# Kernel tuning notes

Measured on AMD Instinct MI355X. Metric: run time of the kernel, lower is better.

## Reference

```python
import jax, jax.numpy as jnp
import numpy as np

L = 32          # ss_num: number of sampled layers
D = 512         # lstm_size
OPS = 16        # operations_num
TEMP = 5.0
TANH_C = 2.5
OP_TANH_RED = 2.5
NEG = jnp.float32(-1e9)  # finite mask value (avoids inf/nan in grads)


def setup_inputs() -> dict:
    key = jax.random.key(0)
    ks = jax.random.split(key, 9)
    u = lambda k, s: jax.random.uniform(k, s, jnp.float32, -0.1, 0.1)  # reset_param: uniform(-0.1, 0.1)
    return {
        "embedding": u(ks[0], (OPS + 1, D)),
        "w_ih": u(ks[1], (4 * D, D)),
        "w_hh": u(ks[2], (4 * D, D)),
        "b_ih": u(ks[3], (4 * D,)),
        "b_hh": u(ks[4], (4 * D,)),
        "w_attn_1": u(ks[5], (D, D)),
        "w_attn_2": u(ks[6], (D, D)),
        "index_fc": u(ks[7], (D,)),
        "op_fc": u(ks[8], (OPS, D)),
    }


def _lstm_cell(x, h, c, w_ih, w_hh, b_ih, b_hh):
    # torch.nn.LSTMCell: gate order i, f, g, o
    g = x @ w_ih.T + b_ih + h @ w_hh.T + b_hh
    i, f, gg, o = jnp.split(g, 4, axis=-1)
    c2 = jax.nn.sigmoid(f) * c + jax.nn.sigmoid(i) * jnp.tanh(gg)
    h2 = jax.nn.sigmoid(o) * jnp.tanh(c2)
    return h2, c2


def reference(embedding, w_ih, w_hh, b_ih, b_hh, w_attn_1, w_attn_2, index_fc, op_fc):
    cell = lambda x, h, c: _lstm_cell(x, h, c, w_ih, w_hh, b_ih, b_hh)
    skey = jax.random.key(42)

    # --- initial construct_node (prev state = zeros) ---
    inp0 = embedding[OPS]                 # embedding of sentinel token [D]
    h, c = cell(inp0, jnp.zeros((D,), jnp.float32), jnp.zeros((D,), jnp.float32))
    anchors = jnp.zeros((L + 1, D), jnp.float32)            # anchor[0] = zeros_like(h)
    anchors_w1 = jnp.zeros((L + 1, D), jnp.float32).at[0].set(h @ w_attn_1.T)

    def step(carry, t):
        h, c, inp, anchors, anchors_w1, key = carry
        k1, k2, key = jax.random.split(key, 3)
        valid = jnp.arange(L + 1) <= t  # anchors 0..t exist at layer t

        # node selection
        h, c = cell(inp, h, c)
        query = jnp.tanh(anchors_w1 + h @ w_attn_2.T)        # [L+1, D]
        idx_logits = (query @ index_fc) / TEMP               # [L+1]
        idx_logits = TANH_C * jnp.tanh(idx_logits)
        idx_logits = jnp.where(valid, idx_logits, NEG)
        node_idx = jax.random.categorical(k1, idx_logits)
        lsm = jax.nn.log_softmax(idx_logits)
        node_lp = -lsm[node_idx]                             # cross_entropy
        node_ent = -jnp.sum(jnp.where(valid, lsm, 0.0) * jnp.exp(lsm))

        # op selection
        op_in = anchors[node_idx]
        h, c = cell(op_in, h, c)
        op_logits = (h @ op_fc.T) / TEMP
        op_logits = (TANH_C / OP_TANH_RED) * jnp.tanh(op_logits)
        op_idx = jax.random.categorical(k2, op_logits)
        olsm = jax.nn.log_softmax(op_logits)
        op_lp = -olsm[op_idx]
        op_ent = -jnp.sum(olsm * jnp.exp(olsm))

        inp = embedding[op_idx]
        anchors = anchors.at[t + 1].set(h)
        anchors_w1 = anchors_w1.at[t + 1].set(h @ w_attn_1.T)
        ent = jax.lax.stop_gradient(node_ent + op_ent)       # entropy is .detach()ed
        return (h, c, inp, anchors, anchors_w1, key), (node_idx, op_idx, node_lp + op_lp, ent)

    carry0 = (h, c, inp0, anchors, anchors_w1, skey)
    _, (nidx, oidx, lps, ents) = jax.lax.scan(step, carry0, jnp.arange(L))
    arch_seq = jnp.stack([nidx, oidx], axis=1).reshape(-1)   # interleave [node, op] x L
    return arch_seq, jnp.sum(ents), jnp.sum(lps)
```

## Files before the change

### kernel.cpp

```cpp
#include <hip/hip_runtime.h>
#include <stdint.h>


#define KWG    64
#define NTH    512
#define LSTEPS 32
#define DDIM   512
#define NOPS   16
#define NEGC   (-1.0e9f)

static __device__ __forceinline__ void tf2x32(uint32_t k0, uint32_t k1,
                                              uint32_t c0, uint32_t c1,
                                              uint32_t& o0, uint32_t& o1){
  uint32_t ks2 = k0 ^ k1 ^ 0x1BD11BDAu;
  uint32_t x0 = c0 + k0;
  uint32_t x1 = c1 + k1;
#define TFR(r) { x0 += x1; x1 = (x1 << (r)) | (x1 >> (32 - (r))); x1 ^= x0; }
  TFR(13) TFR(15) TFR(26) TFR(6)
  x0 += k1;  x1 += ks2 + 1u;
  TFR(17) TFR(29) TFR(16) TFR(24)
  x0 += ks2; x1 += k0 + 2u;
  TFR(13) TFR(15) TFR(26) TFR(6)
  x0 += k0;  x1 += k1 + 3u;
  TFR(17) TFR(29) TFR(16) TFR(24)
  x0 += k1;  x1 += ks2 + 4u;
  TFR(13) TFR(15) TFR(26) TFR(6)
  x0 += ks2; x1 += k0 + 5u;
#undef TFR
  o0 = x0; o1 = x1;
}

static __device__ __forceinline__ float gumbel_bits(uint32_t bits){
  float f = __uint_as_float((bits >> 9) | 0x3f800000u) - 1.0f;
  float u = (f == 0.0f) ? 1.1754943508222875e-38f : f;
  return -logf(-logf(u));
}

static __device__ __forceinline__ float sigm(float x){
  return 1.0f / (1.0f + expf(-x));
}

static __device__ __forceinline__ float wredsum(float v){
  #pragma unroll
  for (int m = 32; m; m >>= 1) v += __shfl_xor(v, m, 64);
  return v;
}

static __device__ __forceinline__ void gl8(const float* __restrict__ p, int lane, float* r){
  #pragma unroll
  for (int k = 0; k < 8; ++k) r[k] = p[(k << 6) + lane];
}

static __device__ __forceinline__ float dot8(const float* w, const float* x){
  float s = 0.f;
  #pragma unroll
  for (int k = 0; k < 8; ++k) s += w[k]*x[k];
  return s;
}

static __device__ __forceinline__ uint64_t tpack(uint32_t tag, float f){
  return ((uint64_t)tag << 32) | (uint64_t)__float_as_uint(f);
}
static __device__ __forceinline__ uint64_t ald64(const uint64_t* p){
  return __hip_atomic_load(p, __ATOMIC_RELAXED, __HIP_MEMORY_SCOPE_AGENT);
}
static __device__ __forceinline__ void ast64(uint64_t* p, uint64_t v){
  __hip_atomic_store(p, v, __ATOMIC_RELAXED, __HIP_MEMORY_SCOPE_AGENT);
}
static __device__ __forceinline__ float poll1(const uint64_t* p, uint32_t tag){
  uint64_t v = ald64(p);
  while ((uint32_t)(v >> 32) != tag){
    __builtin_amdgcn_s_sleep(1);
    v = ald64(p);
  }
  return __uint_as_float((uint32_t)v);
}
static __device__ __forceinline__ void poll8s(const uint64_t* base, int lane,
                                              uint32_t tag, float* r){
  uint64_t v[8];
  for (;;){
    #pragma unroll
    for (int k = 0; k < 8; ++k) v[k] = ald64(base + (k << 6) + lane);
    bool ok = true;
    #pragma unroll
    for (int k = 0; k < 8; ++k) ok &= ((uint32_t)(v[k] >> 32) == tag);
    if (ok) break;
    __builtin_amdgcn_s_sleep(1);
  }
  #pragma unroll
  for (int k = 0; k < 8; ++k) r[k] = __uint_as_float((uint32_t)v[k]);
}

__global__ void __launch_bounds__(NTH, 2)
Controller_60601988547087_kernel(const float* __restrict__ emb,
                                 const float* __restrict__ wih,
                                 const float* __restrict__ whh,
                                 const float* __restrict__ bih,
                                 const float* __restrict__ bhh,
                                 const float* __restrict__ wa1,
                                 const float* __restrict__ wa2,
                                 const float* __restrict__ idxfc,
                                 const float* __restrict__ opfc,
                                 float* __restrict__ out,
                                 uint64_t* __restrict__ ws64)
{
  const int tid  = threadIdx.x;
  const int wg   = blockIdx.x;
  const int wave = tid >> 6;
  const int lane = tid & 63;
  const int unit = (wg << 3) | wave;

  uint64_t* bufA64 = ws64;
  uint64_t* bufB64 = ws64 + 512;
  uint64_t* hw2g64 = ws64 + 1024;
  uint64_t* aw1g64 = ws64 + 1536;
  uint64_t* cand64 = ws64 + 1536 + 32*512;

  __shared__ float s_hc[DDIM];
  __shared__ float s_h1[DDIM];
  __shared__ float s_hw2[DDIM];
  __shared__ float s_xproj[17 * 32];
  __shared__ float s_aproj[33 * 33];
  __shared__ float s_opfc[NOPS * DDIM];
  __shared__ float s_logits[33];
  __shared__ float s_oplog[16];
  __shared__ int   s_ibc[2];

  float wihr[4][8], whhr[4][8], a1r[8], a2r[8], fcr[8], bsum[4];
  #pragma unroll
  for (int g = 0; g < 4; ++g){
    gl8(wih + (size_t)((g << 9) + unit) * DDIM, lane, wihr[g]);
    gl8(whh + (size_t)((g << 9) + unit) * DDIM, lane, whhr[g]);
    bsum[g] = bih[(g << 9) + unit] + bhh[(g << 9) + unit];
  }
  gl8(wa1 + (size_t)unit * DDIM, lane, a1r);
  gl8(wa2 + (size_t)unit * DDIM, lane, a2r);
  gl8(idxfc, lane, fcr);

  for (int i = tid; i < NOPS * DDIM; i += NTH) s_opfc[i] = opfc[i];
  if (tid < 33) s_aproj[tid] = 0.0f;

  for (int op = 0; op <= NOPS; ++op){
    float xc[8];
    gl8(emb + (size_t)op * DDIM, lane, xc);
    #pragma unroll
    for (int g = 0; g < 4; ++g){
      float xp = wredsum(dot8(wihr[g], xc));
      if (lane == 0) s_xproj[op * 32 + (wave << 2) + g] = xp;
    }
  }
  __syncthreads();

  float row0[8], row1[8], row2[8], row3[8];

  float cst;
  {
    const float* xp = s_xproj + 16 * 32 + (wave << 2);
    float gi = sigm(xp[0] + bsum[0]);
    float go = sigm(xp[3] + bsum[3]);
    cst = gi * tanhf(xp[2] + bsum[2]);
    float h0 = go * tanhf(cst);
    if (lane == 0) ast64(bufB64 + unit, tpack(1u, h0));
  }
  s_hc[tid] = poll1(bufB64 + tid, 1u);
  __syncthreads();

  uint32_t key0 = 0u, key1v = 42u;
  float ent_sum = 0.f, lp_sum = 0.f;
  int prev_op = NOPS;

  for (int t = 0; t < LSTEPS; ++t){
    const uint32_t tagA = 3u*(uint32_t)t + 2u;
    const uint32_t tagB = 3u*(uint32_t)t + 3u;
    const uint32_t tagK = 3u*(uint32_t)t + 4u;

    float hc8[8];
    gl8(s_hc, lane, hc8);

    {
      const float* xp = s_xproj + prev_op * 32 + (wave << 2);
      float p0 = wredsum(dot8(whhr[0], hc8));
      float p1 = wredsum(dot8(whhr[1], hc8));
      float p2 = wredsum(dot8(whhr[2], hc8));
      float p3 = wredsum(dot8(whhr[3], hc8));
      float gi = sigm(xp[0] + p0 + bsum[0]);
      float gf = sigm(xp[1] + p1 + bsum[1]);
      float go = sigm(xp[3] + p3 + bsum[3]);
      cst = gf * cst + gi * tanhf(xp[2] + p2 + bsum[2]);
      float hn = go * tanhf(cst);
      if (lane == 0) ast64(bufA64 + unit, tpack(tagA, hn));
    }
    {
      float pa = wredsum(dot8(a1r, hc8));
      if (lane == 0) ast64(aw1g64 + (size_t)t * DDIM + unit, tpack(tagA, pa));
      if (t > 0){
        #pragma unroll
        for (int g = 0; g < 4; ++g){
          float ap = wredsum(dot8(wihr[g], hc8));
          if (lane == 0) s_aproj[t * 33 + (wave << 2) + g] = ap;
        }
      }
    }
    if (wave == (t & 7)){
      const uint64_t* rb = aw1g64 + (size_t)t * DDIM;
      int slot = t >> 3;
      if      (slot == 0) poll8s(rb, lane, tagA, row0);
      else if (slot == 1) poll8s(rb, lane, tagA, row1);
      else if (slot == 2) poll8s(rb, lane, tagA, row2);
      else                poll8s(rb, lane, tagA, row3);
    }
    s_h1[tid] = poll1(bufA64 + tid, tagA);
    __syncthreads();

    float h18[8];
    gl8(s_h1, lane, h18);
    {
      float q = wredsum(dot8(a2r, h18));
      if (lane == 0) ast64(hw2g64 + unit, tpack(tagB, q));
    }
    float ghh0 = wredsum(dot8(whhr[0], h18));
    float ghh1 = wredsum(dot8(whhr[1], h18));
    float ghh2 = wredsum(dot8(whhr[2], h18));
    float ghh3 = wredsum(dot8(whhr[3], h18));
    float cst_cand = 0.f;
    if (lane <= t){
      const float* ag = s_aproj + lane * 33 + (wave << 2);
      float gi = sigm(ag[0] + ghh0 + bsum[0]);
      float gf = sigm(ag[1] + ghh1 + bsum[1]);
      float go = sigm(ag[3] + ghh3 + bsum[3]);
      cst_cand = gf * cst + gi * tanhf(ag[2] + ghh2 + bsum[2]);
      float h2c = go * tanhf(cst_cand);
      ast64(cand64 + (size_t)lane * DDIM + unit, tpack(tagK, h2c));
    }
    s_hw2[tid] = poll1(hw2g64 + tid, tagB);
    __syncthreads();

    int ni;
    float nlp_s = 0.f, nent_s = 0.f;
    uint32_t k2a_s = 0u, k2b_s = 0u;
    {
      float h2c[8];
      gl8(s_hw2, lane, h2c);
#define ROWDOT(RR, I)                                                          \
      { int i_ = (I);                                                          \
        if (i_ <= t){                                                          \
          float acc = 0.f;                                                     \
          _Pragma("unroll")                                                    \
          for (int k = 0; k < 8; ++k) acc += tanhf(RR[k] + h2c[k]) * fcr[k];   \
          acc = wredsum(acc);                                                  \
          if (lane == 0) s_logits[i_] = 2.5f * tanhf(acc / 5.0f);              \
        } }
      ROWDOT(row0, wave)
      ROWDOT(row1, wave + 8)
      ROWDOT(row2, wave + 16)
      ROWDOT(row3, wave + 24)
#undef ROWDOT
      __syncthreads();
      if (wave == 0){
        uint32_t s0 = 0, s1 = 0;
        if (lane < 3) tf2x32(key0, key1v, 0u, (uint32_t)lane, s0, s1);
        uint32_t k1a = __shfl(s0, 0, 64), k1b = __shfl(s1, 0, 64);
        k2a_s = __shfl(s0, 1, 64); k2b_s = __shfl(s1, 1, 64);
        uint32_t nk0 = __shfl(s0, 2, 64), nk1 = __shfl(s1, 2, 64);
        key0 = nk0; key1v = nk1;
        uint32_t y0 = 0, y1 = 0;
        if (lane < 33) tf2x32(k1a, k1b, 0u, (uint32_t)lane, y0, y1);
        uint32_t bits = y0 ^ y1;
        float gmb   = gumbel_bits(bits);
        float logit = (lane < 33) ? ((lane <= t) ? s_logits[lane] : NEGC) : -3.0e38f;
        float cand  = (lane < 33) ? (logit + gmb) : -3.0e38f;
        float v = cand; int bi = lane;
        #pragma unroll
        for (int m = 32; m; m >>= 1){
          float ov = __shfl_xor(v, m, 64); int ob = __shfl_xor(bi, m, 64);
          if (ov > v || (ov == v && ob < bi)){ v = ov; bi = ob; }
        }
        int ni_ = bi;
        float lm = (lane < 33) ? logit : -3.0e38f;
        #pragma unroll
        for (int m = 32; m; m >>= 1) lm = fmaxf(lm, __shfl_xor(lm, m, 64));
        float ex   = (lane < 33) ? expf(logit - lm) : 0.f;
        float ssum = wredsum(ex);
        float lsm  = logit - lm - logf(ssum);
        nlp_s  = -__shfl(lsm, ni_, 64);
        float entc = (lane <= t) ? (-lsm * expf(lsm)) : 0.f;
        nent_s = wredsum(entc);
        if (lane == 0) s_ibc[0] = ni_;
      }
      __syncthreads();
      ni = s_ibc[0];
    }

    cst = __shfl(cst_cand, ni, 64);
    s_hc[tid] = poll1(cand64 + (size_t)ni * DDIM + tid, tagK);
    __syncthreads();

    {
      float h28[8];
      gl8(s_hc, lane, h28);
      #pragma unroll
      for (int jj = 0; jj < 2; ++jj){
        int i = wave + (jj << 3);
        float acc = 0.f;
        #pragma unroll
        for (int k = 0; k < 8; ++k) acc += s_opfc[i * DDIM + (k << 6) + lane] * h28[k];
        acc = wredsum(acc);
        if (lane == 0) s_oplog[i] = tanhf(acc / 5.0f);
      }
      __syncthreads();
    }
    int oi;
    {
      if (wave == 0){
        uint32_t z0 = 0, z1 = 0;
        if (lane < 16) tf2x32(k2a_s, k2b_s, 0u, (uint32_t)lane, z0, z1);
        uint32_t bits = z0 ^ z1;
        float gmb   = gumbel_bits(bits);
        float logit = (lane < 16) ? s_oplog[lane] : -3.0e38f;
        float cand  = (lane < 16) ? (logit + gmb) : -3.0e38f;
        float v = cand; int bi = lane;
        #pragma unroll
        for (int m = 32; m; m >>= 1){
          float ov = __shfl_xor(v, m, 64); int ob = __shfl_xor(bi, m, 64);
          if (ov > v || (ov == v && ob < bi)){ v = ov; bi = ob; }
        }
        int oi_ = bi;
        float lm = (lane < 16) ? logit : -3.0e38f;
        #pragma unroll
        for (int m = 32; m; m >>= 1) lm = fmaxf(lm, __shfl_xor(lm, m, 64));
        float ex   = (lane < 16) ? expf(logit - lm) : 0.f;
        float ssum = wredsum(ex);
        float olsm = logit - lm - logf(ssum);
        float olp  = -__shfl(olsm, oi_, 64);
        float oent = wredsum((lane < 16) ? (-olsm * expf(olsm)) : 0.f);
        lp_sum  += nlp_s + olp;
        ent_sum += nent_s + oent;
        if (lane == 0){
          s_ibc[1] = oi_;
          if (wg == 0){
            out[2 * t]     = (float)ni;
            out[2 * t + 1] = (float)oi_;
          }
        }
      }
      __syncthreads();
      oi = s_ibc[1];
    }
    prev_op = oi;
  }

  if (wg == 0 && wave == 0 && lane == 0){
    out[64] = ent_sum;
    out[65] = lp_sum;
  }
}

extern "C" void kernel_launch(void* const* d_in, const int* in_sizes, int n_in,
                              void* d_out, int out_size, void* d_ws, size_t ws_size,
                              hipStream_t stream) {
  (void)in_sizes; (void)n_in; (void)out_size; (void)ws_size;
  const float* emb  = (const float*)d_in[0];
  const float* wih  = (const float*)d_in[1];
  const float* whh  = (const float*)d_in[2];
  const float* bih  = (const float*)d_in[3];
  const float* bhh  = (const float*)d_in[4];
  const float* wa1  = (const float*)d_in[5];
  const float* wa2  = (const float*)d_in[6];
  const float* ifc  = (const float*)d_in[7];
  const float* ofc  = (const float*)d_in[8];
  float* out = (float*)d_out;
  uint64_t* ws = (uint64_t*)d_ws;
  hipLaunchKernelGGL(Controller_60601988547087_kernel,
                     dim3(KWG), dim3(NTH), 0, stream,
                     emb, wih, whh, bih, bhh, wa1, wa2, ifc, ofc, out, ws);
}
```

Before: 418.4 us.

## Speculate next-step LSTM cell for all 17 possible ops before op sampling

Moves the first LSTM cell of step t+1 ahead of op selection at step t. Each unit computes the candidate hidden state for every one of the 17 possible previous ops, using a transposed xproj table, and publishes them. Once the op is sampled, the matching candidate is simply polled. This removes one grid-wide dependent LSTM-plus-exchange phase from the serial critical path of each step. In exchange it adds candidate stores and a larger workspace, and the per-step tag scheme changes.

```diff
diff --git a/kernel.cpp b/kernel.cpp
--- a/kernel.cpp
+++ b/kernel.cpp
@@ -110,16 +110,17 @@
   const int lane = tid & 63;
   const int unit = (wg << 3) | wave;
 
-  uint64_t* bufA64 = ws64;
-  uint64_t* bufB64 = ws64 + 512;
-  uint64_t* hw2g64 = ws64 + 1024;
-  uint64_t* aw1g64 = ws64 + 1536;
-  uint64_t* cand64 = ws64 + 1536 + 32*512;
+  uint64_t* h1c64  = ws64;
+  uint64_t* hw2g64 = ws64 + 17*512;
+  uint64_t* aw1g64 = ws64 + 18*512;
+  uint64_t* cand64 = ws64 + 50*512;
+  uint64_t* buf064 = cand64 + 32*512;
 
   __shared__ float s_hc[DDIM];
   __shared__ float s_h1[DDIM];
   __shared__ float s_hw2[DDIM];
   __shared__ float s_xproj[17 * 32];
+  __shared__ float s_xprojT[32 * 17];
   __shared__ float s_aproj[33 * 33];
   __shared__ float s_opfc[NOPS * DDIM];
   __shared__ float s_logits[33];
@@ -146,7 +147,10 @@
     #pragma unroll
     for (int g = 0; g < 4; ++g){
       float xp = wredsum(dot8(wihr[g], xc));
-      if (lane == 0) s_xproj[op * 32 + (wave << 2) + g] = xp;
+      if (lane == 0){
+        s_xproj [op * 32 + (wave << 2) + g] = xp;
+        s_xprojT[((wave << 2) + g) * 17 + op] = xp;
+      }
     }
   }
   __syncthreads();
@@ -160,56 +164,55 @@
     float go = sigm(xp[3] + bsum[3]);
     cst = gi * tanhf(xp[2] + bsum[2]);
     float h0 = go * tanhf(cst);
-    if (lane == 0) ast64(bufB64 + unit, tpack(1u, h0));
-  }
-  s_hc[tid] = poll1(bufB64 + tid, 1u);
+    if (lane == 0) ast64(buf064 + unit, tpack(1u, h0));
+  }
+  s_hc[tid] = poll1(buf064 + tid, 1u);
   __syncthreads();
+
+  float cst1_cand = 0.f;
+  {
+    float hc8[8];
+    gl8(s_hc, lane, hc8);
+    float p0 = wredsum(dot8(whhr[0], hc8));
+    float p1 = wredsum(dot8(whhr[1], hc8));
+    float p2 = wredsum(dot8(whhr[2], hc8));
+    float p3 = wredsum(dot8(whhr[3], hc8));
+    if (lane < 17){
+      const float* xt = s_xprojT;
+      int w4 = (wave << 2);
+      float x0 = xt[(w4+0)*17 + lane], x1 = xt[(w4+1)*17 + lane];
+      float x2 = xt[(w4+2)*17 + lane], x3 = xt[(w4+3)*17 + lane];
+      float gi = sigm(x0 + p0 + bsum[0]);
+      float gf = sigm(x1 + p1 + bsum[1]);
+      float go = sigm(x3 + p3 + bsum[3]);
+      cst1_cand = gf * cst + gi * tanhf(x2 + p2 + bsum[2]);
+      float h1v = go * tanhf(cst1_cand);
+      ast64(h1c64 + (size_t)lane * DDIM + unit, tpack(1u, h1v));
+    }
+    float pa = wredsum(dot8(a1r, hc8));
+    if (lane == 0) ast64(aw1g64 + unit, tpack(1u, pa));
+  }
 
   uint32_t key0 = 0u, key1v = 42u;
   float ent_sum = 0.f, lp_sum = 0.f;
   int prev_op = NOPS;
 
   for (int t = 0; t < LSTEPS; ++t){
-    const uint32_t tagA = 3u*(uint32_t)t + 2u;
-    const uint32_t tagB = 3u*(uint32_t)t + 3u;
-    const uint32_t tagK = 3u*(uint32_t)t + 4u;
-
-    float hc8[8];
-    gl8(s_hc, lane, hc8);
-
-    {
-      const float* xp = s_xproj + prev_op * 32 + (wave << 2);
-      float p0 = wredsum(dot8(whhr[0], hc8));
-      float p1 = wredsum(dot8(whhr[1], hc8));
-      float p2 = wredsum(dot8(whhr[2], hc8));
-      float p3 = wredsum(dot8(whhr[3], hc8));
-      float gi = sigm(xp[0] + p0 + bsum[0]);
-      float gf = sigm(xp[1] + p1 + bsum[1]);
-      float go = sigm(xp[3] + p3 + bsum[3]);
-      cst = gf * cst + gi * tanhf(xp[2] + p2 + bsum[2]);
-      float hn = go * tanhf(cst);
-      if (lane == 0) ast64(bufA64 + unit, tpack(tagA, hn));
-    }
-    {
-      float pa = wredsum(dot8(a1r, hc8));
-      if (lane == 0) ast64(aw1g64 + (size_t)t * DDIM + unit, tpack(tagA, pa));
-      if (t > 0){
-        #pragma unroll
-        for (int g = 0; g < 4; ++g){
-          float ap = wredsum(dot8(wihr[g], hc8));
-          if (lane == 0) s_aproj[t * 33 + (wave << 2) + g] = ap;
-        }
-      }
-    }
+    const uint32_t tagH  = 4u*(uint32_t)t + 1u;
+    const uint32_t tagB  = 4u*(uint32_t)t + 2u;
+    const uint32_t tagK  = 4u*(uint32_t)t + 3u;
+    const uint32_t tagH2 = 4u*(uint32_t)t + 5u;
+
+    cst = __shfl(cst1_cand, prev_op, 64);
     if (wave == (t & 7)){
       const uint64_t* rb = aw1g64 + (size_t)t * DDIM;
       int slot = t >> 3;
-      if      (slot == 0) poll8s(rb, lane, tagA, row0);
-      else if (slot == 1) poll8s(rb, lane, tagA, row1);
-      else if (slot == 2) poll8s(rb, lane, tagA, row2);
-      else                poll8s(rb, lane, tagA, row3);
-    }
-    s_h1[tid] = poll1(bufA64 + tid, tagA);
+      if      (slot == 0) poll8s(rb, lane, tagH, row0);
+      else if (slot == 1) poll8s(rb, lane, tagH, row1);
+      else if (slot == 2) poll8s(rb, lane, tagH, row2);
+      else                poll8s(rb, lane, tagH, row3);
+    }
+    s_h1[tid] = poll1(h1c64 + (size_t)prev_op * DDIM + tid, tagH);
     __syncthreads();
 
     float h18[8];
@@ -222,14 +225,14 @@
     float ghh1 = wredsum(dot8(whhr[1], h18));
     float ghh2 = wredsum(dot8(whhr[2], h18));
     float ghh3 = wredsum(dot8(whhr[3], h18));
-    float cst_cand = 0.f;
+    float cst2_cand = 0.f;
     if (lane <= t){
       const float* ag = s_aproj + lane * 33 + (wave << 2);
       float gi = sigm(ag[0] + ghh0 + bsum[0]);
       float gf = sigm(ag[1] + ghh1 + bsum[1]);
       float go = sigm(ag[3] + ghh3 + bsum[3]);
-      cst_cand = gf * cst + gi * tanhf(ag[2] + ghh2 + bsum[2]);
-      float h2c = go * tanhf(cst_cand);
+      cst2_cand = gf * cst + gi * tanhf(ag[2] + ghh2 + bsum[2]);
+      float h2c = go * tanhf(cst2_cand);
       ast64(cand64 + (size_t)lane * DDIM + unit, tpack(tagK, h2c));
     }
     s_hw2[tid] = poll1(hw2g64 + tid, tagB);
@@ -291,19 +294,44 @@
       ni = s_ibc[0];
     }
 
-    cst = __shfl(cst_cand, ni, 64);
+    cst = __shfl(cst2_cand, ni, 64);
     s_hc[tid] = poll1(cand64 + (size_t)ni * DDIM + tid, tagK);
     __syncthreads();
 
+    float hc8[8];
+    gl8(s_hc, lane, hc8);
+    if (t < LSTEPS - 1){
+      float p0 = wredsum(dot8(whhr[0], hc8));
+      float p1 = wredsum(dot8(whhr[1], hc8));
+      float p2 = wredsum(dot8(whhr[2], hc8));
+      float p3 = wredsum(dot8(whhr[3], hc8));
+      if (lane < 17){
+        const float* xt = s_xprojT;
+        int w4 = (wave << 2);
+        float x0 = xt[(w4+0)*17 + lane], x1 = xt[(w4+1)*17 + lane];
+        float x2 = xt[(w4+2)*17 + lane], x3 = xt[(w4+3)*17 + lane];
+        float gi = sigm(x0 + p0 + bsum[0]);
+        float gf = sigm(x1 + p1 + bsum[1]);
+        float go = sigm(x3 + p3 + bsum[3]);
+        cst1_cand = gf * cst + gi * tanhf(x2 + p2 + bsum[2]);
+        float h1v = go * tanhf(cst1_cand);
+        ast64(h1c64 + (size_t)lane * DDIM + unit, tpack(tagH2, h1v));
+      }
+      float pa = wredsum(dot8(a1r, hc8));
+      if (lane == 0) ast64(aw1g64 + (size_t)(t + 1) * DDIM + unit, tpack(tagH2, pa));
+      #pragma unroll
+      for (int g = 0; g < 4; ++g){
+        float ap = wredsum(dot8(wihr[g], hc8));
+        if (lane == 0) s_aproj[(t + 1) * 33 + (wave << 2) + g] = ap;
+      }
+    }
     {
-      float h28[8];
-      gl8(s_hc, lane, h28);
       #pragma unroll
       for (int jj = 0; jj < 2; ++jj){
         int i = wave + (jj << 3);
         float acc = 0.f;
         #pragma unroll
-        for (int k = 0; k < 8; ++k) acc += s_opfc[i * DDIM + (k << 6) + lane] * h28[k];
+        for (int k = 0; k < 8; ++k) acc += s_opfc[i * DDIM + (k << 6) + lane] * hc8[k];
         acc = wredsum(acc);
         if (lane == 0) s_oplog[i] = tanhf(acc / 5.0f);
       }
```

After: 424.3 us. No clear change (+1.4%).
